# Optimization experiments

Hardware: AMD Instinct MI355X
Metric: run time of the kernel (lower is better)

The kernel has to match this reference:

```python
import jax, jax.numpy as jnp
import numpy as np

N_FRAMES = 250
SAMPLE_RATE = 44100
LOWEST_HZ = 55.0
COEFF_VEC_SIZE = int(SAMPLE_RATE // LOWEST_HZ) + 2  # 803 = IIR buffer size / max order
N_SAMPLES = 131072
BURST_LEN = 2048


def _spline_coeffs(t, x):
    """Natural cubic spline coeffs, torchcubicspline convention. t:(n,), x:(n,c)."""
    n = t.shape[0]
    h = t[1:] - t[:-1]
    hinv = 1.0 / h
    hinv2 = hinv * hinv
    dx3 = 3.0 * (x[1:] - x[:-1])                      # 3 * path diffs, (n-1, c)
    rhs_part = dx3 * hinv2[:, None]
    diag = 2.0 * (jnp.zeros(n, t.dtype).at[:-1].add(hinv).at[1:].add(hinv))
    rhs = jnp.zeros_like(x).at[:-1].add(rhs_part).at[1:].add(rhs_part)
    # Tridiagonal system for knot first-derivatives; n is small (n_frames) so a
    # dense solve is clean, differentiable and cheap.
    M = jnp.diag(diag) + jnp.diag(hinv, 1) + jnp.diag(hinv, -1)
    k = jnp.linalg.solve(M, rhs)                      # knot derivatives, (n, c)
    hc = hinv[:, None]
    a = x[:-1]
    b = k[:-1]
    two_c = (2.0 * dx3 * hc - 4.0 * k[:-1] - 2.0 * k[1:]) * hc
    three_d = (-2.0 * dx3 * hc + 3.0 * (k[:-1] + k[1:])) * hc * hc
    return a, b, two_c, three_d


def _spline_eval(t_knots, coeffs, t_out):
    a, b, two_c, three_d = coeffs
    idx = jnp.clip(jnp.searchsorted(t_knots, t_out, side='left') - 1,
                   0, t_knots.shape[0] - 2)
    f = (t_out - t_knots[idx])[:, None]
    inner = b[idx] + (0.5 * two_c[idx] + three_d[idx] * (f / 3.0)) * f
    return a[idx] + inner * f


def setup_inputs() -> dict:
    key = jax.random.key(0)
    k1, k2, k3 = jax.random.split(key, 3)
    # delay in [100, 300) samples -> fundamental 147-441 Hz, safely < buffer 803
    delay = 100.0 + 200.0 * jax.random.uniform(k1, (N_FRAMES,), dtype=jnp.float32)
    # raw reflection-coeff logits, uniform in coeff_range = (-2, 0)
    raw = jax.random.uniform(k2, (N_FRAMES, 2), dtype=jnp.float32,
                             minval=-2.0, maxval=0.0)
    exc = jax.random.normal(k3, (BURST_LEN,), dtype=jnp.float32)
    return {"delay_len_frames": delay, "raw_coeff_frames": raw,
            "excitation": exc, "n_samples": N_SAMPLES}


def reference(delay_len_frames, raw_coeff_frames, excitation, n_samples):
    # constrained coefficients: sigmoid then normalize so b1 + b2 == 1
    sig = jax.nn.sigmoid(raw_coeff_frames)
    coeff_frames = sig / jnp.sum(sig, axis=-1, keepdims=True)          # (F, 2)

    # upsample frame-rate params to sample rate with natural cubic splines
    t_in = jnp.linspace(0.0, 1.0, N_FRAMES)
    t_out = jnp.linspace(0.0, 1.0, n_samples)
    delay = _spline_eval(t_in, _spline_coeffs(t_in, delay_len_frames[:, None]),
                         t_out)[:, 0]                                  # (N,)
    coeffs = _spline_eval(t_in, _spline_coeffs(t_in, coeff_frames), t_out)  # (N, 2)

    zf = jnp.floor(delay)
    z = zf.astype(jnp.int32)              # taps sit at lags z+1, z+2, z+3
    alfa = delay - zf                     # fractional part (grad flows to delay)
    b1, b2 = coeffs[:, 0], coeffs[:, 1]
    g1 = b1 * (1.0 - alfa)                # = -A[t, z]
    g2 = b1 * alfa + b2 * (1.0 - alfa)    # = -A[t, z+1]
    g3 = b2 * alfa                        # = -A[t, z+2]

    x = jnp.zeros(n_samples, excitation.dtype).at[:excitation.shape[0]].set(excitation)

    # sample_wise_lpc: y[t] = x[t] - sum_i A[t, i] * y[t-1-i].
    # A has exactly 3 nonzeros per row, so run the sparse recursion with a
    # ring buffer of size COEFF_VEC_SIZE instead of a dense (N, 803) dot.
    L = COEFF_VEC_SIZE
    buf0 = jnp.zeros(L, x.dtype)
    ts = jnp.arange(n_samples, dtype=jnp.int32)

    def step(buf, inp):
        t, xt, zt, a1, a2, a3 = inp
        y = (xt
             + a1 * buf[(t - zt - 1) % L]
             + a2 * buf[(t - zt - 2) % L]
             + a3 * buf[(t - zt - 3) % L])
        buf = buf.at[t % L].set(y)
        return buf, y

    _, y = jax.lax.scan(step, buf0, (ts, x, z, g1, g2, g3))
    return y
```

## Files before the change

### kernel.cpp

```cpp
#include <hip/hip_runtime.h>
#include <math.h>

#define POFF 128

__global__ void __launch_bounds__(256)
spline_setup(const float* __restrict__ delay_in,
             const float* __restrict__ raw,
             double* __restrict__ coef,
             int* __restrict__ minz,
             int* __restrict__ chunkmin,
             int nChTot, int nf) {
    __shared__ double xch[3 * 256];
    __shared__ double Aa[2][512], Ab[2][512], Ac[2][512];
    __shared__ double Ad0[2][512], Ad1[2][512], Ad2[2][512];

    const int tid = threadIdx.x;
    if (tid == 0) *minz = 0x7fffffff;
    for (int i = tid; i < nChTot; i += 256) chunkmin[i] = 0x7fffffff;

    #pragma unroll
    for (int b = 0; b < 2; ++b)
        for (int i = tid; i < 512; i += 256) {
            Aa[b][i] = 0.0; Ab[b][i] = 1.0; Ac[b][i] = 0.0;
            Ad0[b][i] = 0.0; Ad1[b][i] = 0.0; Ad2[b][i] = 0.0;
        }

    if (tid < nf) {
        double s0 = 1.0 / (1.0 + exp(-(double)raw[2 * tid + 0]));
        double s1 = 1.0 / (1.0 + exp(-(double)raw[2 * tid + 1]));
        double ss = s0 + s1;
        xch[0 * 256 + tid] = (double)delay_in[tid];
        xch[1 * 256 + tid] = s0 / ss;
        xch[2 * 256 + tid] = s1 / ss;
    }
    __syncthreads();

    if (tid < nf) {
        int i = tid;
        double hinv = (double)(nf - 1);
        Aa[0][POFF + i] = (i > 0) ? 1.0 : 0.0;
        Ac[0][POFF + i] = (i < nf - 1) ? 1.0 : 0.0;
        Ab[0][POFF + i] = (i == 0 || i == nf - 1) ? 2.0 : 4.0;
        #pragma unroll
        for (int ch = 0; ch < 3; ++ch) {
            const double* x = xch + ch * 256;
            double r = 0.0;
            if (i < nf - 1) r += 3.0 * hinv * (x[i + 1] - x[i]);
            if (i > 0)      r += 3.0 * hinv * (x[i] - x[i - 1]);
            if (ch == 0) Ad0[0][POFF + i] = r;
            else if (ch == 1) Ad1[0][POFF + i] = r;
            else Ad2[0][POFF + i] = r;
        }
    }
    __syncthreads();

    int cur = 0;
    for (int s = 1; s < nf; s <<= 1) {
        int nxt = cur ^ 1;
        int ic = POFF + tid, im = ic - s, ip = ic + s;
        double ai = Aa[cur][ic], bi = Ab[cur][ic], ci = Ac[cur][ic];
        double alpha = -ai / Ab[cur][im];
        double gamma = -ci / Ab[cur][ip];
        double na = alpha * Aa[cur][im];
        double nc = gamma * Ac[cur][ip];
        double nb = bi + alpha * Ac[cur][im] + gamma * Aa[cur][ip];
        double n0 = Ad0[cur][ic] + alpha * Ad0[cur][im] + gamma * Ad0[cur][ip];
        double n1 = Ad1[cur][ic] + alpha * Ad1[cur][im] + gamma * Ad1[cur][ip];
        double n2 = Ad2[cur][ic] + alpha * Ad2[cur][im] + gamma * Ad2[cur][ip];
        Aa[nxt][ic] = na; Ab[nxt][ic] = nb; Ac[nxt][ic] = nc;
        Ad0[nxt][ic] = n0; Ad1[nxt][ic] = n1; Ad2[nxt][ic] = n2;
        cur = nxt;
        __syncthreads();
    }

    int nint = nf - 1;
    double hinv = (double)(nf - 1);
    if (tid < nint) {
        int i = tid;
        double rbI = 1.0 / Ab[cur][POFF + i], rbI1 = 1.0 / Ab[cur][POFF + i + 1];
        #pragma unroll
        for (int ch = 0; ch < 3; ++ch) {
            double ki, ki1;
            if (ch == 0) { ki = Ad0[cur][POFF + i] * rbI; ki1 = Ad0[cur][POFF + i + 1] * rbI1; }
            else if (ch == 1) { ki = Ad1[cur][POFF + i] * rbI; ki1 = Ad1[cur][POFF + i + 1] * rbI1; }
            else { ki = Ad2[cur][POFF + i] * rbI; ki1 = Ad2[cur][POFF + i + 1] * rbI1; }
            const double* x = xch + ch * 256;
            double dx3 = 3.0 * (x[i + 1] - x[i]);
            double two_c   = (2.0 * dx3 * hinv - 4.0 * ki - 2.0 * ki1) * hinv;
            double three_d = (-2.0 * dx3 * hinv + 3.0 * (ki + ki1)) * hinv * hinv;
            double* C = coef + (size_t)(ch * nint + i) * 4;
            C[0] = x[i];
            C[1] = ki;
            C[2] = 0.5 * two_c;
            C[3] = three_d * (1.0 / 3.0);
        }
    }
}

__global__ void eval_kernel(const double* __restrict__ coef,
                            float4* __restrict__ gx,
                            int* __restrict__ minz,
                            int* __restrict__ chunkmin,
                            int n, int nTot, int nf) {
    int j = blockIdx.x * blockDim.x + threadIdx.x;
    if (j >= nTot) return;
    if (j >= n) { gx[j] = make_float4(0.f, 0.f, 0.f, 0.f); return; }

    double u = (double)j / (double)(n - 1);
    double nfm1 = (double)(nf - 1);
    int idx = (int)(u * nfm1);
    if (idx > nf - 2) idx = nf - 2;
    if (idx < 0) idx = 0;
    double tknot = (double)idx / nfm1;
    if (u < tknot && idx > 0) {
        idx--; tknot = (double)idx / nfm1;
    } else {
        double tnext = (double)(idx + 1) / nfm1;
        if (u >= tnext && idx < nf - 2) { idx++; tknot = tnext; }
    }
    double f = u - tknot;

    int nint = nf - 1;
    const double* C0 = coef + (size_t)(0 * nint + idx) * 4;
    const double* C1 = coef + (size_t)(1 * nint + idx) * 4;
    const double* C2 = coef + (size_t)(2 * nint + idx) * 4;
    double dly = C0[0] + f * (C0[1] + f * (C0[2] + f * C0[3]));
    double b1d = C1[0] + f * (C1[1] + f * (C1[2] + f * C1[3]));
    double b2d = C2[0] + f * (C2[1] + f * (C2[2] + f * C2[3]));

    double zf = floor(dly);
    int z = (int)zf;
    float alfa = (float)(dly - zf);
    float b1 = (float)b1d, b2 = (float)b2d;
    float g1 = b1 * (1.0f - alfa);
    float g2 = b1 * alfa + b2 * (1.0f - alfa);
    float g3 = b2 * alfa;

    int s3 = (j - z - 3) & 2047;
    gx[j] = make_float4(g1, g2, g3, __uint_as_float((unsigned int)s3));

    int wmin = z;
    #pragma unroll
    for (int o = 32; o > 0; o >>= 1) wmin = min(wmin, __shfl_down(wmin, o, 64));
    if ((threadIdx.x & 63) == 0) {
        atomicMin(minz, wmin);
        atomicMin(&chunkmin[j >> 7], wmin);
    }
}

__global__ void __launch_bounds__(128, 1)
scan_kernel(const float4* __restrict__ gx,
            const int* __restrict__ minz,
            const int* __restrict__ chunkmin,
            const float* __restrict__ exc,
            float* __restrict__ y,
            float* __restrict__ sink,
            int n, int burst) {
    __shared__ float buf[2052];
    __shared__ float excl[2048];
    __shared__ __align__(16) int cminL[1024];
    __shared__ float4 ring[4 * 1024];

    const int tid = threadIdx.x;
    for (int i = tid; i < 2052; i += 128) buf[i] = 0.0f;
    for (int i = tid; i < 2048; i += 128) excl[i] = (i < burst) ? exc[i] : 0.0f;
    {
        int nCh = (n + 127) >> 7;
        for (int i = tid; i < 1024; i += 128)
            cminL[i] = (i < nCh) ? chunkmin[i] : 0x7fffffff;
    }

    int mz = __builtin_amdgcn_readfirstlane(*minz);
    const int nFull = n >> 10;

#define GLL(gsrc, ldst)                                                       \
    __builtin_amdgcn_global_load_lds(                                         \
        (const __attribute__((address_space(1))) void*)(gsrc),                \
        (__attribute__((address_space(3))) void*)(ldst), 16, 0, 0)

    if (mz < 63 || nFull < 2) {
        __syncthreads();
        if (tid < 64) {
            int Df = mz + 1;
            if (Df > 64) Df = 64;
            if (Df < 1) Df = 1;
            for (int base = 0; base < n; base += Df) {
                int t = base + tid;
                bool ok = (tid < Df) && (t < n);
                float4 q = ok ? gx[t] : make_float4(0.f, 0.f, 0.f, 0.f);
                unsigned u = __float_as_uint(q.w);
                float a3 = buf[u], a2 = buf[u + 1], a1 = buf[u + 2];
                float x = (t < burst) ? excl[t & 2047] : 0.0f;
                float y0 = fmaf(q.x, a1, x);
                y0 = fmaf(q.y, a2, y0);
                y0 = fmaf(q.z, a3, y0);
                if (ok) {
                    int w = t & 2047;
                    buf[w] = y0;
                    if (w < 2) buf[2048 + w] = y0;
                    y[t] = y0;
                }
            }
        }
        return;
    }

    if (tid >= 64) {
        int lane = tid - 64;
        #pragma unroll
        for (int c = 0; c < 16; ++c)
            GLL(gx + (c << 6) + lane, &ring[(c << 6)]);
        #pragma unroll
        for (int c = 0; c < 16; ++c)
            GLL(gx + 1024 + (c << 6) + lane, &ring[1024 + (c << 6)]);
    }
    __syncthreads();

    for (int g = 0; g < nFull; ++g) {
        if (tid >= 64) {
            int lane = tid - 64;
            int prevw = ((g - 1) & 1) << 10;
            int prev = (g - 1) << 10;
            float vals[16];
            #pragma unroll
            for (int k = 0; k < 16; ++k)
                vals[k] = buf[prevw + (k << 6) + lane];
            #pragma unroll
            for (int k = 0; k < 16; ++k) {
                int off = (k << 6) + lane;
                float* dst = (g > 0) ? (y + prev + off) : (sink + off);
                *dst = vals[k];
            }
            int pb = (g + 2) << 10;
            int slot = (g + 2) & 3;
            #pragma unroll
            for (int c = 0; c < 16; ++c)
                GLL(gx + pb + (c << 6) + lane, &ring[(slot << 10) + (c << 6)]);
            asm volatile("s_waitcnt vmcnt(32)" ::: "memory");
        } else {
            const float4* Rp = ring + ((g & 3) << 10);
            int wb = ((g & 1) << 10) + tid;
            int gb = g << 10;
            bool wx = (gb < burst);
            int g8 = g << 3;
            int4 fa = *(const int4*)&cminL[g8];
            int4 fb = *(const int4*)&cminL[g8 + 4];
            int fl[8] = { fa.x, fa.y, fa.z, fa.w, fb.x, fb.y, fb.z, fb.w };
            float4 q0 = Rp[tid];
            float4 q1 = Rp[64 + tid];
            #pragma unroll
            for (int c = 0; c < 8; ++c) {
                float4 p0, p1;
                if (c < 7) {
                    p0 = Rp[((c + 1) << 7) + tid];
                    p1 = Rp[((c + 1) << 7) + 64 + tid];
                }
                float x0 = 0.0f, x1 = 0.0f;
                if (wx) {
                    int t = gb + (c << 7) + tid;
                    x0 = (t < burst) ? excl[t & 2047] : 0.0f;
                    int t1 = t + 64;
                    x1 = (t1 < burst) ? excl[t1 & 2047] : 0.0f;
                }
                if (__builtin_amdgcn_readfirstlane(fl[c]) >= 127) {
                    unsigned u0 = __float_as_uint(q0.w);
                    unsigned u1 = __float_as_uint(q1.w);
                    float a3 = buf[u0], a2 = buf[u0 + 1], a1 = buf[u0 + 2];
                    float b3 = buf[u1], b2 = buf[u1 + 1], b1 = buf[u1 + 2];
                    float y0 = fmaf(q0.x, a1, x0);
                    y0 = fmaf(q0.y, a2, y0);
                    y0 = fmaf(q0.z, a3, y0);
                    float y1 = fmaf(q1.x, b1, x1);
                    y1 = fmaf(q1.y, b2, y1);
                    y1 = fmaf(q1.z, b3, y1);
                    buf[wb + (c << 7)] = y0;
                    buf[wb + (c << 7) + 64] = y1;
                    if (c == 0 && (g & 1) == 0 && tid < 2) buf[2048 + tid] = y0;
                } else {
                    unsigned u0 = __float_as_uint(q0.w);
                    float a3 = buf[u0], a2 = buf[u0 + 1], a1 = buf[u0 + 2];
                    float y0 = fmaf(q0.x, a1, x0);
                    y0 = fmaf(q0.y, a2, y0);
                    y0 = fmaf(q0.z, a3, y0);
                    buf[wb + (c << 7)] = y0;
                    if (c == 0 && (g & 1) == 0 && tid < 2) buf[2048 + tid] = y0;
                    unsigned u1 = __float_as_uint(q1.w);
                    float b3 = buf[u1], b2 = buf[u1 + 1], b1 = buf[u1 + 2];
                    float y1 = fmaf(q1.x, b1, x1);
                    y1 = fmaf(q1.y, b2, y1);
                    y1 = fmaf(q1.z, b3, y1);
                    buf[wb + (c << 7) + 64] = y1;
                }
                q0 = p0; q1 = p1;
            }
        }
        asm volatile("s_waitcnt lgkmcnt(0)" ::: "memory");
        __builtin_amdgcn_sched_barrier(0);
        __builtin_amdgcn_s_barrier();
        __builtin_amdgcn_sched_barrier(0);
    }

    __syncthreads();

    if (tid >= 64) {
        int lane = tid - 64;
        int start = (nFull - 1) << 10;
        #pragma unroll
        for (int k = 0; k < 16; ++k) {
            int t = start + (k << 6) + lane;
            if (t < n) y[t] = buf[t & 2047];
        }
    } else {
        for (int base = nFull << 10; base < n; base += 64) {
            int t = base + tid;
            bool ok = (t < n);
            float4 q = ok ? gx[t] : make_float4(0.f, 0.f, 0.f, 0.f);
            unsigned u = __float_as_uint(q.w);
            float a3 = buf[u], a2 = buf[u + 1], a1 = buf[u + 2];
            float x = (t < burst) ? excl[t & 2047] : 0.0f;
            float y0 = fmaf(q.x, a1, x);
            y0 = fmaf(q.y, a2, y0);
            y0 = fmaf(q.z, a3, y0);
            if (ok) {
                int w = t & 2047;
                buf[w] = y0;
                if (w < 2) buf[2048 + w] = y0;
                y[t] = y0;
            }
        }
    }
#undef GLL
}

extern "C" void kernel_launch(void* const* d_in, const int* in_sizes, int n_in,
                              void* d_out, int out_size, void* d_ws, size_t ws_size,
                              hipStream_t stream) {
    const float* delay = (const float*)d_in[0];
    const float* raw   = (const float*)d_in[1];
    const float* exc   = (const float*)d_in[2];
    int nf = in_sizes[0];
    int burst = in_sizes[2];
    if (burst > 2048) burst = 2048;
    int n = out_size;
    int nTot = n + 4096;
    int nChTot = (nTot + 127) >> 7;

    char* ws = (char*)d_ws;
    size_t coefBytes = (size_t)3 * (nf - 1) * 4 * sizeof(double);
    size_t off = (coefBytes + 255) & ~(size_t)255;
    double* coef = (double*)ws;
    int* minz = (int*)(ws + off);
    off += 256;
    int* chunkmin = (int*)(ws + off);
    off += 8192;
    float* sink = (float*)(ws + off);
    off += 4096;
    float4* gxa = (float4*)(ws + off);

    spline_setup<<<1, 256, 0, stream>>>(delay, raw, coef, minz, chunkmin, nChTot, nf);
    eval_kernel<<<(nTot + 255) / 256, 256, 0, stream>>>(coef, gxa, minz, chunkmin, n, nTot, nf);
    scan_kernel<<<1, 128, 0, stream>>>(gxa, minz, chunkmin, exc, (float*)d_out, sink, n, burst);
}
```

Baseline: 183.9 us.

## Pick scan wavefront width from analytic spline minimum delay, templated per width

The spline setup now computes the minimum delay analytically over each cubic segment and reduces it to a global lower bound. The scan kernel uses that bound to choose a step width of 64 to 128 samples, picking a ring buffer size to match, and instantiates a templated scan body per width. This replaces the per-chunk runtime minimum checks and the fixed 64-wide processing. More samples can then be resolved per serial step when delays are long, at the cost of a non-power-of-two modulo buffer and more code paths. A per-sample atomic minimum is still kept to validate the analytic bound before the fast path is taken.

```diff
diff --git a/kernel.cpp b/kernel.cpp
--- a/kernel.cpp
+++ b/kernel.cpp
@@ -1,22 +1,33 @@
 #include <hip/hip_runtime.h>
 #include <math.h>
+#include <float.h>
 
 #define POFF 128
+
+__device__ __forceinline__ int select_D(int mz) {
+    int dmax = mz + 1;
+    if (dmax >= 128) return 128;
+    if (dmax >= 112) return 112;
+    if (dmax >= 96)  return 96;
+    if (dmax >= 80)  return 80;
+    return 64;
+}
+__device__ __forceinline__ int m_of(int D) { return (D == 64) ? 2048 : 16 * D; }
 
 __global__ void __launch_bounds__(256)
 spline_setup(const float* __restrict__ delay_in,
              const float* __restrict__ raw,
              double* __restrict__ coef,
              int* __restrict__ minz,
-             int* __restrict__ chunkmin,
-             int nChTot, int nf) {
+             int nf) {
     __shared__ double xch[3 * 256];
     __shared__ double Aa[2][512], Ab[2][512], Ac[2][512];
     __shared__ double Ad0[2][512], Ad1[2][512], Ad2[2][512];
+    __shared__ double dmin[256];
 
     const int tid = threadIdx.x;
-    if (tid == 0) *minz = 0x7fffffff;
-    for (int i = tid; i < nChTot; i += 256) chunkmin[i] = 0x7fffffff;
+    if (tid == 0) minz[1] = 0x7fffffff;
+    dmin[tid] = DBL_MAX;
 
     #pragma unroll
     for (int b = 0; b < 2; ++b)
@@ -93,18 +104,50 @@
             C[1] = ki;
             C[2] = 0.5 * two_c;
             C[3] = three_d * (1.0 / 3.0);
-        }
-    }
+            if (ch == 0) {
+                double a = x[i], b = ki;
+                double C2 = 0.5 * two_c, C3 = three_d * (1.0 / 3.0);
+                double h = 1.0 / hinv;
+                double m = fmin(a, a + h * (b + h * (C2 + h * C3)));
+                double A = three_d, B = two_c;
+                if (fabs(A) > 1e-30) {
+                    double disc = B * B - 4.0 * A * b;
+                    if (disc >= 0.0) {
+                        double sq = sqrt(disc);
+                        double r1 = (-B + sq) / (2.0 * A);
+                        double r2 = (-B - sq) / (2.0 * A);
+                        if (r1 > 0.0 && r1 < h)
+                            m = fmin(m, a + r1 * (b + r1 * (C2 + r1 * C3)));
+                        if (r2 > 0.0 && r2 < h)
+                            m = fmin(m, a + r2 * (b + r2 * (C2 + r2 * C3)));
+                    }
+                } else if (fabs(B) > 1e-30) {
+                    double r = -b / B;
+                    if (r > 0.0 && r < h)
+                        m = fmin(m, a + r * (b + r * (C2 + r * C3)));
+                }
+                dmin[i] = m;
+            }
+        }
+    }
+    __syncthreads();
+    #pragma unroll
+    for (int s = 128; s > 0; s >>= 1) {
+        if (tid < s) dmin[tid] = fmin(dmin[tid], dmin[tid + s]);
+        __syncthreads();
+    }
+    if (tid == 0) minz[0] = (int)floor(dmin[0]);
 }
 
 __global__ void eval_kernel(const double* __restrict__ coef,
                             float4* __restrict__ gx,
                             int* __restrict__ minz,
-                            int* __restrict__ chunkmin,
                             int n, int nTot, int nf) {
     int j = blockIdx.x * blockDim.x + threadIdx.x;
     if (j >= nTot) return;
     if (j >= n) { gx[j] = make_float4(0.f, 0.f, 0.f, 0.f); return; }
+
+    int M = m_of(select_D(minz[0]));
 
     double u = (double)j / (double)(n - 1);
     double nfm1 = (double)(nf - 1);
@@ -136,54 +179,193 @@
     float g2 = b1 * alfa + b2 * (1.0f - alfa);
     float g3 = b2 * alfa;
 
-    int s3 = (j - z - 3) & 2047;
+    int s3 = (j - z - 3) % M;
+    if (s3 < 0) s3 += M;
     gx[j] = make_float4(g1, g2, g3, __uint_as_float((unsigned int)s3));
 
     int wmin = z;
     #pragma unroll
     for (int o = 32; o > 0; o >>= 1) wmin = min(wmin, __shfl_down(wmin, o, 64));
-    if ((threadIdx.x & 63) == 0) {
-        atomicMin(minz, wmin);
-        atomicMin(&chunkmin[j >> 7], wmin);
+    if ((threadIdx.x & 63) == 0) atomicMin(&minz[1], wmin);
+}
+
+#define GLLm(gsrc, ldst)                                                      \
+    __builtin_amdgcn_global_load_lds(                                         \
+        (const __attribute__((address_space(1))) void*)(gsrc),                \
+        (__attribute__((address_space(3))) void*)(ldst), 16, 0, 0)
+
+template<int D>
+__device__ __forceinline__ void scan_body(const float4* __restrict__ gx,
+                                          float* __restrict__ y,
+                                          float* __restrict__ sink,
+                                          int n, int burst, int tid,
+                                          float (&buf)[2052], float (&excl)[2048],
+                                          float4 (&ring)[4096]) {
+    constexpr int NC   = (D == 64) ? 16 : 8;
+    constexpr int ROWS = (D == 64) ? 1 : 2;
+    constexpr int CST  = (D == 64) ? 64 : 128;
+    constexpr int SPAN = NC * D;
+    constexpr int M    = 2 * SPAN;
+    constexpr int NP   = SPAN / 64;
+    const int nFull = n / SPAN;
+
+    if (tid >= 64) {
+        int lane = tid - 64;
+        #pragma unroll
+        for (int c = 0; c < NC; ++c) {
+            GLLm(gx + c * D + lane, &ring[c * CST]);
+            if constexpr (ROWS == 2) GLLm(gx + c * D + 64 + lane, &ring[c * CST + 64]);
+        }
+        #pragma unroll
+        for (int c = 0; c < NC; ++c) {
+            GLLm(gx + SPAN + c * D + lane, &ring[1024 + c * CST]);
+            if constexpr (ROWS == 2) GLLm(gx + SPAN + c * D + 64 + lane, &ring[1024 + c * CST + 64]);
+        }
+    }
+    __syncthreads();
+
+    for (int g = 0; g < nFull; ++g) {
+        if (tid >= 64) {
+            int lane = tid - 64;
+            int prevw = ((g - 1) & 1) ? SPAN : 0;
+            int prev = (g - 1) * SPAN;
+            float vals[NP];
+            #pragma unroll
+            for (int k = 0; k < NP; ++k)
+                vals[k] = buf[prevw + (k << 6) + lane];
+            #pragma unroll
+            for (int k = 0; k < NP; ++k) {
+                int off = (k << 6) + lane;
+                float* dst = (g > 0) ? (y + prev + off) : (sink + off);
+                *dst = vals[k];
+            }
+            int pb = (g + 2) * SPAN;
+            int slot = (g + 2) & 3;
+            #pragma unroll
+            for (int c = 0; c < NC; ++c) {
+                GLLm(gx + pb + c * D + lane, &ring[(slot << 10) + c * CST]);
+                if constexpr (ROWS == 2)
+                    GLLm(gx + pb + c * D + 64 + lane, &ring[(slot << 10) + c * CST + 64]);
+            }
+            if constexpr (NP + 16 == 32) asm volatile("s_waitcnt vmcnt(32)" ::: "memory");
+            else if constexpr (NP + 16 == 30) asm volatile("s_waitcnt vmcnt(30)" ::: "memory");
+            else if constexpr (NP + 16 == 28) asm volatile("s_waitcnt vmcnt(28)" ::: "memory");
+            else if constexpr (NP + 16 == 26) asm volatile("s_waitcnt vmcnt(26)" ::: "memory");
+        } else {
+            const float4* Rp = ring + ((g & 3) << 10);
+            int wb = (((g & 1) ? SPAN : 0)) + tid;
+            int gb = g * SPAN;
+            bool wx = (gb < burst);
+            float4 q0 = Rp[tid];
+            float4 q1;
+            if constexpr (ROWS == 2) q1 = Rp[64 + tid];
+            #pragma unroll
+            for (int c = 0; c < NC; ++c) {
+                float4 p0, p1;
+                if (c < NC - 1) {
+                    p0 = Rp[(c + 1) * CST + tid];
+                    if constexpr (ROWS == 2) p1 = Rp[(c + 1) * CST + 64 + tid];
+                }
+                unsigned u0 = __float_as_uint(q0.w);
+                float a3 = buf[u0], a2 = buf[u0 + 1], a1 = buf[u0 + 2];
+                float x0 = 0.0f, x1 = 0.0f;
+                if (wx) {
+                    int t = gb + c * D + tid;
+                    x0 = (t < burst) ? excl[t & 2047] : 0.0f;
+                    if constexpr (ROWS == 2) {
+                        int t1 = t + 64;
+                        x1 = (t1 < burst) ? excl[t1 & 2047] : 0.0f;
+                    }
+                }
+                float y0 = fmaf(q0.x, a1, x0);
+                y0 = fmaf(q0.y, a2, y0);
+                y0 = fmaf(q0.z, a3, y0);
+                buf[wb + c * D] = y0;
+                if constexpr (ROWS == 2) {
+                    unsigned u1 = __float_as_uint(q1.w);
+                    float b3 = buf[u1], b2 = buf[u1 + 1], b1 = buf[u1 + 2];
+                    float y1 = fmaf(q1.x, b1, x1);
+                    y1 = fmaf(q1.y, b2, y1);
+                    y1 = fmaf(q1.z, b3, y1);
+                    if constexpr (D == 128) {
+                        buf[wb + c * D + 64] = y1;
+                    } else {
+                        if (tid < D - 64) buf[wb + c * D + 64] = y1;
+                    }
+                }
+                if (c == 0 && (g & 1) == 0 && tid < 2) buf[M + tid] = y0;
+                q0 = p0;
+                if constexpr (ROWS == 2) q1 = p1;
+            }
+        }
+        asm volatile("s_waitcnt lgkmcnt(0)" ::: "memory");
+        __builtin_amdgcn_sched_barrier(0);
+        __builtin_amdgcn_s_barrier();
+        __builtin_amdgcn_sched_barrier(0);
+    }
+
+    __syncthreads();
+
+    if (tid >= 64) {
+        int lane = tid - 64;
+        int start = (nFull - 1) * SPAN;
+        int w = ((nFull - 1) & 1) ? SPAN : 0;
+        #pragma unroll
+        for (int k = 0; k < NP; ++k) {
+            int off = (k << 6) + lane;
+            y[start + off] = buf[w + off];
+        }
+    } else {
+        int tb = nFull * SPAN;
+        int wb0 = (nFull & 1) ? SPAN : 0;
+        for (int base = tb; base < n; base += 64) {
+            int t = base + tid;
+            bool ok = (t < n);
+            float4 q = ok ? gx[t] : make_float4(0.f, 0.f, 0.f, 0.f);
+            unsigned u = __float_as_uint(q.w);
+            float a3 = buf[u], a2 = buf[u + 1], a1 = buf[u + 2];
+            float y0 = q.x * a1;
+            y0 = fmaf(q.y, a2, y0);
+            y0 = fmaf(q.z, a3, y0);
+            if (ok) {
+                int w = wb0 + (t - tb);
+                buf[w] = y0;
+                if (w < 2) buf[M + w] = y0;
+                y[t] = y0;
+            }
+        }
     }
 }
 
 __global__ void __launch_bounds__(128, 1)
 scan_kernel(const float4* __restrict__ gx,
             const int* __restrict__ minz,
-            const int* __restrict__ chunkmin,
             const float* __restrict__ exc,
             float* __restrict__ y,
             float* __restrict__ sink,
             int n, int burst) {
     __shared__ float buf[2052];
     __shared__ float excl[2048];
-    __shared__ __align__(16) int cminL[1024];
-    __shared__ float4 ring[4 * 1024];
+    __shared__ float4 ring[4096];
 
     const int tid = threadIdx.x;
     for (int i = tid; i < 2052; i += 128) buf[i] = 0.0f;
     for (int i = tid; i < 2048; i += 128) excl[i] = (i < burst) ? exc[i] : 0.0f;
-    {
-        int nCh = (n + 127) >> 7;
-        for (int i = tid; i < 1024; i += 128)
-            cminL[i] = (i < nCh) ? chunkmin[i] : 0x7fffffff;
-    }
-
-    int mz = __builtin_amdgcn_readfirstlane(*minz);
-    const int nFull = n >> 10;
-
-#define GLL(gsrc, ldst)                                                       \
-    __builtin_amdgcn_global_load_lds(                                         \
-        (const __attribute__((address_space(1))) void*)(gsrc),                \
-        (__attribute__((address_space(3))) void*)(ldst), 16, 0, 0)
-
-    if (mz < 63 || nFull < 2) {
+
+    int mza = __builtin_amdgcn_readfirstlane(minz[0]);
+    int smz = __builtin_amdgcn_readfirstlane(minz[1]);
+    int D = select_D(mza);
+    int M = m_of(D);
+
+    bool fast = (mza >= 63) && (D <= smz + 1) && (n / ((D == 64) ? 1024 : 8 * D)) >= 2;
+
+    if (!fast) {
         __syncthreads();
         if (tid < 64) {
-            int Df = mz + 1;
+            int Df = smz + 1;
             if (Df > 64) Df = 64;
             if (Df < 1) Df = 1;
+            int wb = 0;
             for (int base = 0; base < n; base += Df) {
                 int t = base + tid;
                 bool ok = (tid < Df) && (t < n);
@@ -195,141 +377,26 @@
                 y0 = fmaf(q.y, a2, y0);
                 y0 = fmaf(q.z, a3, y0);
                 if (ok) {
-                    int w = t & 2047;
+                    int w = wb + tid;
+                    if (w >= M) w -= M;
                     buf[w] = y0;
-                    if (w < 2) buf[2048 + w] = y0;
+                    if (w < 2) buf[M + w] = y0;
                     y[t] = y0;
                 }
+                wb += Df;
+                if (wb >= M) wb -= M;
             }
         }
         return;
     }
 
-    if (tid >= 64) {
-        int lane = tid - 64;
-        #pragma unroll
-        for (int c = 0; c < 16; ++c)
-            GLL(gx + (c << 6) + lane, &ring[(c << 6)]);
-        #pragma unroll
-        for (int c = 0; c < 16; ++c)
-            GLL(gx + 1024 + (c << 6) + lane, &ring[1024 + (c << 6)]);
-    }
-    __syncthreads();
-
-    for (int g = 0; g < nFull; ++g) {
-        if (tid >= 64) {
-            int lane = tid - 64;
-            int prevw = ((g - 1) & 1) << 10;
-            int prev = (g - 1) << 10;
-            float vals[16];
-            #pragma unroll
-            for (int k = 0; k < 16; ++k)
-                vals[k] = buf[prevw + (k << 6) + lane];
-            #pragma unroll
-            for (int k = 0; k < 16; ++k) {
-                int off = (k << 6) + lane;
-                float* dst = (g > 0) ? (y + prev + off) : (sink + off);
-                *dst = vals[k];
-            }
-            int pb = (g + 2) << 10;
-            int slot = (g + 2) & 3;
-            #pragma unroll
-            for (int c = 0; c < 16; ++c)
-                GLL(gx + pb + (c << 6) + lane, &ring[(slot << 10) + (c << 6)]);
-            asm volatile("s_waitcnt vmcnt(32)" ::: "memory");
-        } else {
-            const float4* Rp = ring + ((g & 3) << 10);
-            int wb = ((g & 1) << 10) + tid;
-            int gb = g << 10;
-            bool wx = (gb < burst);
-            int g8 = g << 3;
-            int4 fa = *(const int4*)&cminL[g8];
-            int4 fb = *(const int4*)&cminL[g8 + 4];
-            int fl[8] = { fa.x, fa.y, fa.z, fa.w, fb.x, fb.y, fb.z, fb.w };
-            float4 q0 = Rp[tid];
-            float4 q1 = Rp[64 + tid];
-            #pragma unroll
-            for (int c = 0; c < 8; ++c) {
-                float4 p0, p1;
-                if (c < 7) {
-                    p0 = Rp[((c + 1) << 7) + tid];
-                    p1 = Rp[((c + 1) << 7) + 64 + tid];
-                }
-                float x0 = 0.0f, x1 = 0.0f;
-                if (wx) {
-                    int t = gb + (c << 7) + tid;
-                    x0 = (t < burst) ? excl[t & 2047] : 0.0f;
-                    int t1 = t + 64;
-                    x1 = (t1 < burst) ? excl[t1 & 2047] : 0.0f;
-                }
-                if (__builtin_amdgcn_readfirstlane(fl[c]) >= 127) {
-                    unsigned u0 = __float_as_uint(q0.w);
-                    unsigned u1 = __float_as_uint(q1.w);
-                    float a3 = buf[u0], a2 = buf[u0 + 1], a1 = buf[u0 + 2];
-                    float b3 = buf[u1], b2 = buf[u1 + 1], b1 = buf[u1 + 2];
-                    float y0 = fmaf(q0.x, a1, x0);
-                    y0 = fmaf(q0.y, a2, y0);
-                    y0 = fmaf(q0.z, a3, y0);
-                    float y1 = fmaf(q1.x, b1, x1);
-                    y1 = fmaf(q1.y, b2, y1);
-                    y1 = fmaf(q1.z, b3, y1);
-                    buf[wb + (c << 7)] = y0;
-                    buf[wb + (c << 7) + 64] = y1;
-                    if (c == 0 && (g & 1) == 0 && tid < 2) buf[2048 + tid] = y0;
-                } else {
-                    unsigned u0 = __float_as_uint(q0.w);
-                    float a3 = buf[u0], a2 = buf[u0 + 1], a1 = buf[u0 + 2];
-                    float y0 = fmaf(q0.x, a1, x0);
-                    y0 = fmaf(q0.y, a2, y0);
-                    y0 = fmaf(q0.z, a3, y0);
-                    buf[wb + (c << 7)] = y0;
-                    if (c == 0 && (g & 1) == 0 && tid < 2) buf[2048 + tid] = y0;
-                    unsigned u1 = __float_as_uint(q1.w);
-                    float b3 = buf[u1], b2 = buf[u1 + 1], b1 = buf[u1 + 2];
-                    float y1 = fmaf(q1.x, b1, x1);
-                    y1 = fmaf(q1.y, b2, y1);
-                    y1 = fmaf(q1.z, b3, y1);
-                    buf[wb + (c << 7) + 64] = y1;
-                }
-                q0 = p0; q1 = p1;
-            }
-        }
-        asm volatile("s_waitcnt lgkmcnt(0)" ::: "memory");
-        __builtin_amdgcn_sched_barrier(0);
-        __builtin_amdgcn_s_barrier();
-        __builtin_amdgcn_sched_barrier(0);
-    }
-
-    __syncthreads();
-
-    if (tid >= 64) {
-        int lane = tid - 64;
-        int start = (nFull - 1) << 10;
-        #pragma unroll
-        for (int k = 0; k < 16; ++k) {
-            int t = start + (k << 6) + lane;
-            if (t < n) y[t] = buf[t & 2047];
-        }
-    } else {
-        for (int base = nFull << 10; base < n; base += 64) {
-            int t = base + tid;
-            bool ok = (t < n);
-            float4 q = ok ? gx[t] : make_float4(0.f, 0.f, 0.f, 0.f);
-            unsigned u = __float_as_uint(q.w);
-            float a3 = buf[u], a2 = buf[u + 1], a1 = buf[u + 2];
-            float x = (t < burst) ? excl[t & 2047] : 0.0f;
-            float y0 = fmaf(q.x, a1, x);
-            y0 = fmaf(q.y, a2, y0);
-            y0 = fmaf(q.z, a3, y0);
-            if (ok) {
-                int w = t & 2047;
-                buf[w] = y0;
-                if (w < 2) buf[2048 + w] = y0;
-                y[t] = y0;
-            }
-        }
-    }
-#undef GLL
+    switch (D) {
+        case 128: scan_body<128>(gx, y, sink, n, burst, tid, buf, excl, ring); break;
+        case 112: scan_body<112>(gx, y, sink, n, burst, tid, buf, excl, ring); break;
+        case 96:  scan_body<96>(gx, y, sink, n, burst, tid, buf, excl, ring); break;
+        case 80:  scan_body<80 >(gx, y, sink, n, burst, tid, buf, excl, ring); break;
+        default:  scan_body<64 >(gx, y, sink, n, burst, tid, buf, excl, ring); break;
+    }
 }
 
 extern "C" void kernel_launch(void* const* d_in, const int* in_sizes, int n_in,
@@ -343,7 +410,6 @@
     if (burst > 2048) burst = 2048;
     int n = out_size;
     int nTot = n + 4096;
-    int nChTot = (nTot + 127) >> 7;
 
     char* ws = (char*)d_ws;
     size_t coefBytes = (size_t)3 * (nf - 1) * 4 * sizeof(double);
@@ -351,13 +417,11 @@
     double* coef = (double*)ws;
     int* minz = (int*)(ws + off);
     off += 256;
-    int* chunkmin = (int*)(ws + off);
-    off += 8192;
     float* sink = (float*)(ws + off);
     off += 4096;
     float4* gxa = (float4*)(ws + off);
 
-    spline_setup<<<1, 256, 0, stream>>>(delay, raw, coef, minz, chunkmin, nChTot, nf);
-    eval_kernel<<<(nTot + 255) / 256, 256, 0, stream>>>(coef, gxa, minz, chunkmin, n, nTot, nf);
-    scan_kernel<<<1, 128, 0, stream>>>(gxa, minz, chunkmin, exc, (float*)d_out, sink, n, burst);
-}
+    spline_setup<<<1, 256, 0, stream>>>(delay, raw, coef, minz, nf);
+    eval_kernel<<<(nTot + 255) / 256, 256, 0, stream>>>(coef, gxa, minz, n, nTot, nf);
+    scan_kernel<<<1, 128, 0, stream>>>(gxa, minz, exc, (float*)d_out, sink, n, burst);
+}
```

Result: faster. 150.1 us (-18.4%).
